# Performance work log

Measured on AMD Instinct MI355X. Metric: run time of the kernel, lower is better.

## Reference

```python
import jax, jax.numpy as jnp
import numpy as np

L, T, H, F = 16, 2048, 2048, 512  # layers, tokens (B*S=16*128), hidden, features


def setup_inputs() -> dict:
    key = jax.random.key(0)
    k1, k2, k3 = jax.random.split(key, 3)
    x = jax.random.normal(k1, (L, T, H), dtype=jnp.float32)          # stacked residual activations
    W_enc = jax.random.normal(k2, (L, F, H), dtype=jnp.float32) * 0.02  # per-layer encoder (out,in)
    # Dense pack of decoders: W_dec[s, t] is the (source s -> target t) decoder weight (H, F).
    # Only entries with s <= t exist in the original ModuleDict; others are masked to zero in reference().
    W_dec = jax.random.normal(k3, (L, L, H, F), dtype=jnp.float32) * 0.02
    return {"x": x, "W_enc": W_enc, "W_dec": W_dec}


def reference(x, W_enc, W_dec):
    n_layers = x.shape[0]
    # encode: feature_activations[l] = JumpReLU(x[l] @ W_enc[l].T), threshold=0 -> relu
    feats = jax.nn.relu(jnp.einsum('sth,sfh->stf', x, W_enc))  # [L, T, F]
    # causal mask over (source s, target l): decoder exists iff s <= l
    tri = jnp.tril(jnp.ones((n_layers, n_layers), x.dtype))     # tri[l, s] = 1 if s <= l
    Wd = W_dec * tri.T[:, :, None, None]                        # zero out s > l entries
    # reconstruction[l] = sum_{s<=l} feats[s] @ W_dec[s,l].T  (single blocked contraction)
    recon = jnp.einsum('stf,slhf->lth', feats, Wd)              # [L, T, H]
    return feats, recon
```

## Files before the change

kernel.cpp:

```cpp
#include <hip/hip_runtime.h>

#define NL 16
#define NT 2048
#define NH 2048
#define NF 512
#define NPAIR 136

typedef short bf16x8 __attribute__((ext_vector_type(8)));
typedef float f32x4 __attribute__((ext_vector_type(4)));
typedef short s16x4 __attribute__((ext_vector_type(4)));

__device__ __forceinline__ short f2bf(float f) {
  union { float f; unsigned u; } x; x.f = f;
  unsigned r = (x.u + 0x7fffu + ((x.u >> 16) & 1u)) >> 16;
  return (short)r;
}


__global__ void k_cvt_f32_bf16(const float* __restrict__ src, short* __restrict__ dst, int n4) {
  int i = blockIdx.x * blockDim.x + threadIdx.x;
  const int stride = gridDim.x * blockDim.x;
  for (; i < n4; i += stride) {
    const float4 v = reinterpret_cast<const float4*>(src)[i];
    s16x4 o;
    o[0] = f2bf(v.x); o[1] = f2bf(v.y); o[2] = f2bf(v.z); o[3] = f2bf(v.w);
    reinterpret_cast<s16x4*>(dst)[i] = o;
  }
}

__global__ void k_cvt_wdec(const float* __restrict__ wdec, short* __restrict__ dst) {
  const int p = blockIdx.y;
  int l = 0;
  while ((l + 1) * (l + 2) / 2 <= p) ++l;
  const int s = p - l * (l + 1) / 2;
  const float* src = wdec + (size_t)(s * NL + l) * (NH * NF);
  short* d = dst + (size_t)p * (NH * NF);
  const int n4 = NH * NF / 4;
  for (int i = blockIdx.x * blockDim.x + threadIdx.x; i < n4; i += gridDim.x * blockDim.x) {
    const float4 v = reinterpret_cast<const float4*>(src)[i];
    s16x4 o;
    o[0] = f2bf(v.x); o[1] = f2bf(v.y); o[2] = f2bf(v.z); o[3] = f2bf(v.w);
    reinterpret_cast<s16x4*>(d)[i] = o;
  }
}


__device__ __forceinline__ void stage64(const short* gtile, int ld, short* lds, int wave, int lane) {
#pragma unroll
  for (int i = 0; i < 4; ++i) {
    const int row = i * 32 + wave * 8 + (lane >> 3);
    const int col = (lane & 7) * 8;
    __builtin_amdgcn_global_load_lds(
        (const __attribute__((address_space(1))) void*)(gtile + (size_t)row * ld + col),
        (__attribute__((address_space(3))) void*)(lds + i * 2048 + wave * 512),
        16, 0, 0);
  }
}

__device__ __forceinline__ void mma_step(const short* As, const short* Bs,
                                         f32x4 acc[4][4], int wr, int wc, int lane) {
  const int r = lane & 15;
  const int ko = (lane >> 4) * 8;
#pragma unroll
  for (int kk = 0; kk < 2; ++kk) {
    bf16x8 a[4], b[4];
#pragma unroll
    for (int m = 0; m < 4; ++m)
      a[m] = *reinterpret_cast<const bf16x8*>(As + (wr * 64 + m * 16 + r) * 64 + kk * 32 + ko);
#pragma unroll
    for (int n = 0; n < 4; ++n)
      b[n] = *reinterpret_cast<const bf16x8*>(Bs + (wc * 64 + n * 16 + r) * 64 + kk * 32 + ko);
#pragma unroll
    for (int m = 0; m < 4; ++m)
#pragma unroll
      for (int n = 0; n < 4; ++n)
        acc[m][n] = __builtin_amdgcn_mfma_f32_16x16x32_bf16(a[m], b[n], acc[m][n], 0, 0, 0);
  }
}


__global__ __launch_bounds__(256, 2) void k_encode(const short* __restrict__ xbf,
                                                   const short* __restrict__ webf,
                                                   float* __restrict__ feats_f32,
                                                   short* __restrict__ feats_bf) {
  __shared__ short As[128 * 64];
  __shared__ short Bs[128 * 64];
  const int l = blockIdx.z;
  const int row0 = blockIdx.y * 128;
  const int col0 = blockIdx.x * 128;
  const int tid = threadIdx.x;
  const int wave = tid >> 6, lane = tid & 63;
  const int wr = wave >> 1, wc = wave & 1;

  const short* A = xbf + (size_t)l * NT * NH + (size_t)row0 * NH;
  const short* B = webf + (size_t)l * NF * NH + (size_t)col0 * NH;

  f32x4 acc[4][4];
#pragma unroll
  for (int m = 0; m < 4; ++m)
#pragma unroll
    for (int n = 0; n < 4; ++n) {
      f32x4 z = {0.f, 0.f, 0.f, 0.f};
      acc[m][n] = z;
    }

  for (int kt = 0; kt < NH / 64; ++kt) {
    stage64(A + kt * 64, NH, As, wave, lane);
    stage64(B + kt * 64, NH, Bs, wave, lane);
    __syncthreads();
    mma_step(As, Bs, acc, wr, wc, lane);
    __syncthreads();
  }

  const int lr = (lane >> 4) * 4, lc = lane & 15;
  float* outF = feats_f32 + (size_t)l * NT * NF;
  short* outB = feats_bf + (size_t)l * NT * NF;
#pragma unroll
  for (int m = 0; m < 4; ++m) {
#pragma unroll
    for (int n = 0; n < 4; ++n) {
#pragma unroll
      for (int rg = 0; rg < 4; ++rg) {
        const int rr = row0 + wr * 64 + m * 16 + lr + rg;
        const int cc = col0 + wc * 64 + n * 16 + lc;
        float v = acc[m][n][rg];
        v = v > 0.f ? v : 0.f;
        outF[(size_t)rr * NF + cc] = v;
        outB[(size_t)rr * NF + cc] = f2bf(v);
      }
    }
  }
}


__global__ __launch_bounds__(256, 2) void k_decode(const short* __restrict__ featsbf,
                                                   const short* __restrict__ wdbf,
                                                   float* __restrict__ recon) {
  __shared__ short As[128 * 64];
  __shared__ short Bs[128 * 64];
  const int l = (NL - 1) - blockIdx.z;
  const int row0 = blockIdx.y * 128;
  const int col0 = blockIdx.x * 128;
  const int tid = threadIdx.x;
  const int wave = tid >> 6, lane = tid & 63;
  const int wr = wave >> 1, wc = wave & 1;

  f32x4 acc[4][4];
#pragma unroll
  for (int m = 0; m < 4; ++m)
#pragma unroll
    for (int n = 0; n < 4; ++n) {
      f32x4 z = {0.f, 0.f, 0.f, 0.f};
      acc[m][n] = z;
    }

  const int KT = 8 * (l + 1);
  const int pbase = l * (l + 1) / 2;

  for (int kt = 0; kt < KT; ++kt) {
    const int s = kt >> 3;
    const int f0 = (kt & 7) * 64;
    const short* At = featsbf + (size_t)s * NT * NF + (size_t)row0 * NF + f0;
    const short* Bt = wdbf + (size_t)(pbase + s) * NH * NF + (size_t)col0 * NF + f0;
    stage64(At, NF, As, wave, lane);
    stage64(Bt, NF, Bs, wave, lane);
    __syncthreads();
    mma_step(As, Bs, acc, wr, wc, lane);
    __syncthreads();
  }

  const int lr = (lane >> 4) * 4, lc = lane & 15;
  float* out = recon + (size_t)l * NT * NH;
#pragma unroll
  for (int m = 0; m < 4; ++m) {
#pragma unroll
    for (int n = 0; n < 4; ++n) {
#pragma unroll
      for (int rg = 0; rg < 4; ++rg) {
        const int rr = row0 + wr * 64 + m * 16 + lr + rg;
        const int cc = col0 + wc * 64 + n * 16 + lc;
        out[(size_t)rr * NH + cc] = acc[m][n][rg];
      }
    }
  }
}


extern "C" void kernel_launch(void* const* d_in, const int* in_sizes, int n_in,
                              void* d_out, int out_size, void* d_ws, size_t ws_size,
                              hipStream_t stream) {
  const float* x = (const float*)d_in[0];
  const float* wenc = (const float*)d_in[1];
  const float* wdec = (const float*)d_in[2];

  float* feats_f32 = (float*)d_out;
  float* recon = feats_f32 + (size_t)NL * NT * NF;

  short* x_bf = (short*)d_ws;
  short* we_bf = x_bf + (size_t)NL * NT * NH;
  short* wd_bf = we_bf + (size_t)NL * NF * NH;
  short* ft_bf = wd_bf + (size_t)NPAIR * NH * NF;

  k_cvt_f32_bf16<<<2048, 256, 0, stream>>>(x, x_bf, NL * NT * NH / 4);
  k_cvt_f32_bf16<<<2048, 256, 0, stream>>>(wenc, we_bf, NL * NF * NH / 4);
  k_cvt_wdec<<<dim3(512, NPAIR), 256, 0, stream>>>(wdec, wd_bf);

  k_encode<<<dim3(NF / 128, NT / 128, NL), 256, 0, stream>>>(x_bf, we_bf, feats_f32, ft_bf);
  k_decode<<<dim3(NH / 128, NT / 128, NL), 256, 0, stream>>>(ft_bf, wd_bf, recon);
}
```

Baseline: 961.1 us.

## Use 256x256 tiles with double-buffered swizzled LDS pipeline for encode/decode GEMMs

```diff
diff --git a/kernel.cpp b/kernel.cpp
--- a/kernel.cpp
+++ b/kernel.cpp
@@ -15,6 +15,8 @@
   unsigned r = (x.u + 0x7fffu + ((x.u >> 16) & 1u)) >> 16;
   return (short)r;
 }
+
+__device__ __forceinline__ int imin(int a, int b) { return a < b ? a : b; }
 
 
 __global__ void k_cvt_f32_bf16(const float* __restrict__ src, short* __restrict__ dst, int n4) {
@@ -45,144 +47,216 @@
 }
 
 
-__device__ __forceinline__ void stage64(const short* gtile, int ld, short* lds, int wave, int lane) {
-#pragma unroll
-  for (int i = 0; i < 4; ++i) {
-    const int row = i * 32 + wave * 8 + (lane >> 3);
-    const int col = (lane & 7) * 8;
+__device__ __forceinline__ bf16x8 lds_frag(const short* slot, int r, int cbyte) {
+  int byte = (r << 7) + cbyte;
+  byte ^= (r & 7) << 4;
+  return *reinterpret_cast<const bf16x8*>(reinterpret_cast<const char*>(slot) + byte);
+}
+
+__device__ __forceinline__ void stage_half(short* slot, const short* gbase, int ld,
+                                           int isA, int h, int tid, int wave) {
+#pragma unroll
+  for (int j = 0; j < 2; ++j) {
+    const int o = j * 8192 + tid * 16;
+    const int r = o >> 7;
+    const int cb = (o ^ ((r & 7) << 4)) & 127;
+    const int g = isA ? (((r >> 6) << 7) + h * 64 + (r & 63))
+                      : (((r >> 5) << 6) + h * 32 + (r & 31));
     __builtin_amdgcn_global_load_lds(
-        (const __attribute__((address_space(1))) void*)(gtile + (size_t)row * ld + col),
-        (__attribute__((address_space(3))) void*)(lds + i * 2048 + wave * 512),
+        (const __attribute__((address_space(1))) void*)(gbase + (size_t)g * ld + (cb >> 1)),
+        (__attribute__((address_space(3))) void*)((char*)slot + j * 8192 + wave * 1024),
         16, 0, 0);
   }
 }
 
-__device__ __forceinline__ void mma_step(const short* As, const short* Bs,
-                                         f32x4 acc[4][4], int wr, int wc, int lane) {
-  const int r = lane & 15;
-  const int ko = (lane >> 4) * 8;
+template <int QA, int QB, typename StageFn>
+__device__ __forceinline__ void phase(short (*bufc)[8192], f32x4 (&acc)[2][2][4][2],
+                                      int wr, int wc, int lane, StageFn stage) {
+  const int lr = lane & 15;
+  const int ko = (lane >> 4) * 16;
+  bf16x8 af[2][4];
+  bf16x8 bfr[2][2];
 #pragma unroll
   for (int kk = 0; kk < 2; ++kk) {
-    bf16x8 a[4], b[4];
 #pragma unroll
     for (int m = 0; m < 4; ++m)
-      a[m] = *reinterpret_cast<const bf16x8*>(As + (wr * 64 + m * 16 + r) * 64 + kk * 32 + ko);
-#pragma unroll
-    for (int n = 0; n < 4; ++n)
-      b[n] = *reinterpret_cast<const bf16x8*>(Bs + (wc * 64 + n * 16 + r) * 64 + kk * 32 + ko);
+      af[kk][m] = lds_frag(bufc[QA], wr * 64 + m * 16 + lr, kk * 64 + ko);
+#pragma unroll
+    for (int n = 0; n < 2; ++n)
+      bfr[kk][n] = lds_frag(bufc[2 + QB], wc * 32 + n * 16 + lr, kk * 64 + ko);
+  }
+  stage();
+  __builtin_amdgcn_s_barrier();
+  __builtin_amdgcn_s_setprio(1);
+#pragma unroll
+  for (int kk = 0; kk < 2; ++kk)
 #pragma unroll
     for (int m = 0; m < 4; ++m)
 #pragma unroll
-      for (int n = 0; n < 4; ++n)
-        acc[m][n] = __builtin_amdgcn_mfma_f32_16x16x32_bf16(a[m], b[n], acc[m][n], 0, 0, 0);
-  }
-}
-
-
-__global__ __launch_bounds__(256, 2) void k_encode(const short* __restrict__ xbf,
+      for (int n = 0; n < 2; ++n)
+        acc[QA][QB][m][n] = __builtin_amdgcn_mfma_f32_16x16x32_bf16(
+            af[kk][m], bfr[kk][n], acc[QA][QB][m][n], 0, 0, 0);
+  __builtin_amdgcn_s_setprio(0);
+  asm volatile("s_waitcnt vmcnt(8)" ::: "memory");
+  __builtin_amdgcn_s_barrier();
+}
+
+
+__global__ __launch_bounds__(512) void k_encode256(const short* __restrict__ xbf,
                                                    const short* __restrict__ webf,
                                                    float* __restrict__ feats_f32,
                                                    short* __restrict__ feats_bf) {
-  __shared__ short As[128 * 64];
-  __shared__ short Bs[128 * 64];
+  __shared__ short lds[2][4][8192];
   const int l = blockIdx.z;
-  const int row0 = blockIdx.y * 128;
-  const int col0 = blockIdx.x * 128;
+  const int row0 = blockIdx.y * 256;
+  const int col0 = blockIdx.x * 256;
   const int tid = threadIdx.x;
   const int wave = tid >> 6, lane = tid & 63;
-  const int wr = wave >> 1, wc = wave & 1;
+  const int wr = wave >> 2, wc = wave & 3;
 
   const short* A = xbf + (size_t)l * NT * NH + (size_t)row0 * NH;
   const short* B = webf + (size_t)l * NF * NH + (size_t)col0 * NH;
 
-  f32x4 acc[4][4];
-#pragma unroll
-  for (int m = 0; m < 4; ++m)
-#pragma unroll
-    for (int n = 0; n < 4; ++n) {
-      f32x4 z = {0.f, 0.f, 0.f, 0.f};
-      acc[m][n] = z;
-    }
-
-  for (int kt = 0; kt < NH / 64; ++kt) {
-    stage64(A + kt * 64, NH, As, wave, lane);
-    stage64(B + kt * 64, NH, Bs, wave, lane);
-    __syncthreads();
-    mma_step(As, Bs, acc, wr, wc, lane);
-    __syncthreads();
-  }
-
-  const int lr = (lane >> 4) * 4, lc = lane & 15;
+  f32x4 acc[2][2][4][2];
+#pragma unroll
+  for (int qa = 0; qa < 2; ++qa)
+#pragma unroll
+    for (int qb = 0; qb < 2; ++qb)
+#pragma unroll
+      for (int m = 0; m < 4; ++m)
+#pragma unroll
+        for (int n = 0; n < 2; ++n) {
+          f32x4 z = {0.f, 0.f, 0.f, 0.f};
+          acc[qa][qb][m][n] = z;
+        }
+
+  const int KT = NH / 64;
+  stage_half(lds[0][0], A, NH, 1, 0, tid, wave);
+  stage_half(lds[0][2], B, NH, 0, 0, tid, wave);
+  stage_half(lds[0][1], A, NH, 1, 1, tid, wave);
+  stage_half(lds[0][3], B, NH, 0, 1, tid, wave);
+  stage_half(lds[1][0], A + 64, NH, 1, 0, tid, wave);
+  stage_half(lds[1][2], B + 64, NH, 0, 0, tid, wave);
+  asm volatile("s_waitcnt vmcnt(4)" ::: "memory");
+  __builtin_amdgcn_s_barrier();
+
+  for (int u = 0; u < KT; ++u) {
+    short(*bufc)[8192] = lds[u & 1];
+    short(*bufn)[8192] = lds[(u + 1) & 1];
+    phase<0, 0>(bufc, acc, wr, wc, lane, [&] {
+      stage_half(bufn[3], B + imin(u + 1, KT - 1) * 64, NH, 0, 1, tid, wave);
+    });
+    phase<0, 1>(bufc, acc, wr, wc, lane, [&] {
+      stage_half(bufn[1], A + imin(u + 1, KT - 1) * 64, NH, 1, 1, tid, wave);
+    });
+    phase<1, 0>(bufc, acc, wr, wc, lane, [&] {
+      stage_half(bufc[0], A + imin(u + 2, KT - 1) * 64, NH, 1, 0, tid, wave);
+    });
+    phase<1, 1>(bufc, acc, wr, wc, lane, [&] {
+      stage_half(bufc[2], B + imin(u + 2, KT - 1) * 64, NH, 0, 0, tid, wave);
+    });
+  }
+
+  const int lr4 = (lane >> 4) * 4, lc = lane & 15;
   float* outF = feats_f32 + (size_t)l * NT * NF;
   short* outB = feats_bf + (size_t)l * NT * NF;
 #pragma unroll
-  for (int m = 0; m < 4; ++m) {
-#pragma unroll
-    for (int n = 0; n < 4; ++n) {
-#pragma unroll
-      for (int rg = 0; rg < 4; ++rg) {
-        const int rr = row0 + wr * 64 + m * 16 + lr + rg;
-        const int cc = col0 + wc * 64 + n * 16 + lc;
-        float v = acc[m][n][rg];
-        v = v > 0.f ? v : 0.f;
-        outF[(size_t)rr * NF + cc] = v;
-        outB[(size_t)rr * NF + cc] = f2bf(v);
-      }
-    }
-  }
-}
-
-
-__global__ __launch_bounds__(256, 2) void k_decode(const short* __restrict__ featsbf,
+  for (int qa = 0; qa < 2; ++qa)
+#pragma unroll
+    for (int qb = 0; qb < 2; ++qb)
+#pragma unroll
+      for (int m = 0; m < 4; ++m)
+#pragma unroll
+        for (int n = 0; n < 2; ++n)
+#pragma unroll
+          for (int rg = 0; rg < 4; ++rg) {
+            const int rr = row0 + wr * 128 + qa * 64 + m * 16 + lr4 + rg;
+            const int cc = col0 + wc * 64 + qb * 32 + n * 16 + lc;
+            float v = acc[qa][qb][m][n][rg];
+            v = v > 0.f ? v : 0.f;
+            outF[(size_t)rr * NF + cc] = v;
+            outB[(size_t)rr * NF + cc] = f2bf(v);
+          }
+}
+
+
+__global__ __launch_bounds__(512) void k_decode256(const short* __restrict__ featsbf,
                                                    const short* __restrict__ wdbf,
                                                    float* __restrict__ recon) {
-  __shared__ short As[128 * 64];
-  __shared__ short Bs[128 * 64];
-  const int l = (NL - 1) - blockIdx.z;
-  const int row0 = blockIdx.y * 128;
-  const int col0 = blockIdx.x * 128;
+  __shared__ short lds[2][4][8192];
+  const int zg = blockIdx.z >> 2, zi = blockIdx.z & 3;
+  const int l = (zi < 2) ? (15 - 2 * zg - zi) : (2 * zg + 3 - zi);
+  const int row0 = blockIdx.y * 256;
+  const int col0 = blockIdx.x * 256;
   const int tid = threadIdx.x;
   const int wave = tid >> 6, lane = tid & 63;
-  const int wr = wave >> 1, wc = wave & 1;
-
-  f32x4 acc[4][4];
-#pragma unroll
-  for (int m = 0; m < 4; ++m)
-#pragma unroll
-    for (int n = 0; n < 4; ++n) {
-      f32x4 z = {0.f, 0.f, 0.f, 0.f};
-      acc[m][n] = z;
-    }
+  const int wr = wave >> 2, wc = wave & 3;
+  const int pbase = l * (l + 1) / 2;
+
+  const short* Af = featsbf + (size_t)row0 * NF;
+  const short* Bw = wdbf + (size_t)col0 * NF;
+
+  f32x4 acc[2][2][4][2];
+#pragma unroll
+  for (int qa = 0; qa < 2; ++qa)
+#pragma unroll
+    for (int qb = 0; qb < 2; ++qb)
+#pragma unroll
+      for (int m = 0; m < 4; ++m)
+#pragma unroll
+        for (int n = 0; n < 2; ++n) {
+          f32x4 z = {0.f, 0.f, 0.f, 0.f};
+          acc[qa][qb][m][n] = z;
+        }
 
   const int KT = 8 * (l + 1);
-  const int pbase = l * (l + 1) / 2;
-
-  for (int kt = 0; kt < KT; ++kt) {
-    const int s = kt >> 3;
-    const int f0 = (kt & 7) * 64;
-    const short* At = featsbf + (size_t)s * NT * NF + (size_t)row0 * NF + f0;
-    const short* Bt = wdbf + (size_t)(pbase + s) * NH * NF + (size_t)col0 * NF + f0;
-    stage64(At, NF, As, wave, lane);
-    stage64(Bt, NF, Bs, wave, lane);
-    __syncthreads();
-    mma_step(As, Bs, acc, wr, wc, lane);
-    __syncthreads();
-  }
-
-  const int lr = (lane >> 4) * 4, lc = lane & 15;
+#define ABASE(kt) (Af + (size_t)((kt) >> 3) * (NT * NF) + ((kt)&7) * 64)
+#define BBASE(kt) (Bw + (size_t)(pbase + ((kt) >> 3)) * (NH * NF) + ((kt)&7) * 64)
+
+  stage_half(lds[0][0], ABASE(0), NF, 1, 0, tid, wave);
+  stage_half(lds[0][2], BBASE(0), NF, 0, 0, tid, wave);
+  stage_half(lds[0][1], ABASE(0), NF, 1, 1, tid, wave);
+  stage_half(lds[0][3], BBASE(0), NF, 0, 1, tid, wave);
+  stage_half(lds[1][0], ABASE(1), NF, 1, 0, tid, wave);
+  stage_half(lds[1][2], BBASE(1), NF, 0, 0, tid, wave);
+  asm volatile("s_waitcnt vmcnt(4)" ::: "memory");
+  __builtin_amdgcn_s_barrier();
+
+  for (int u = 0; u < KT; ++u) {
+    short(*bufc)[8192] = lds[u & 1];
+    short(*bufn)[8192] = lds[(u + 1) & 1];
+    phase<0, 0>(bufc, acc, wr, wc, lane, [&] {
+      stage_half(bufn[3], BBASE(imin(u + 1, KT - 1)), NF, 0, 1, tid, wave);
+    });
+    phase<0, 1>(bufc, acc, wr, wc, lane, [&] {
+      stage_half(bufn[1], ABASE(imin(u + 1, KT - 1)), NF, 1, 1, tid, wave);
+    });
+    phase<1, 0>(bufc, acc, wr, wc, lane, [&] {
+      stage_half(bufc[0], ABASE(imin(u + 2, KT - 1)), NF, 1, 0, tid, wave);
+    });
+    phase<1, 1>(bufc, acc, wr, wc, lane, [&] {
+      stage_half(bufc[2], BBASE(imin(u + 2, KT - 1)), NF, 0, 0, tid, wave);
+    });
+  }
+#undef ABASE
+#undef BBASE
+
+  const int lr4 = (lane >> 4) * 4, lc = lane & 15;
   float* out = recon + (size_t)l * NT * NH;
 #pragma unroll
-  for (int m = 0; m < 4; ++m) {
-#pragma unroll
-    for (int n = 0; n < 4; ++n) {
-#pragma unroll
-      for (int rg = 0; rg < 4; ++rg) {
-        const int rr = row0 + wr * 64 + m * 16 + lr + rg;
-        const int cc = col0 + wc * 64 + n * 16 + lc;
-        out[(size_t)rr * NH + cc] = acc[m][n][rg];
-      }
-    }
-  }
+  for (int qa = 0; qa < 2; ++qa)
+#pragma unroll
+    for (int qb = 0; qb < 2; ++qb)
+#pragma unroll
+      for (int m = 0; m < 4; ++m)
+#pragma unroll
+        for (int n = 0; n < 2; ++n)
+#pragma unroll
+          for (int rg = 0; rg < 4; ++rg) {
+            const int rr = row0 + wr * 128 + qa * 64 + m * 16 + lr4 + rg;
+            const int cc = col0 + wc * 64 + qb * 32 + n * 16 + lc;
+            out[(size_t)rr * NH + cc] = acc[qa][qb][m][n][rg];
+          }
 }
 
 
@@ -205,6 +279,6 @@
   k_cvt_f32_bf16<<<2048, 256, 0, stream>>>(wenc, we_bf, NL * NF * NH / 4);
   k_cvt_wdec<<<dim3(512, NPAIR), 256, 0, stream>>>(wdec, wd_bf);
 
-  k_encode<<<dim3(NF / 128, NT / 128, NL), 256, 0, stream>>>(x_bf, we_bf, feats_f32, ft_bf);
-  k_decode<<<dim3(NH / 128, NT / 128, NL), 256, 0, stream>>>(ft_bf, wd_bf, recon);
-}
+  k_encode256<<<dim3(2, 8, 16), 512, 0, stream>>>(x_bf, we_bf, feats_f32, ft_bf);
+  k_decode256<<<dim3(8, 8, 16), 512, 0, stream>>>(ft_bf, wd_bf, recon);
+}
```

Measured after the change: 911.8 us. 1.05x faster.

## Use 256x256 tiles with 32x32 MFMA and a multi-stage LDS prefetch ring

Applied to the files above, without the earlier changes.

```diff
diff --git a/kernel.cpp b/kernel.cpp
--- a/kernel.cpp
+++ b/kernel.cpp
@@ -7,7 +7,7 @@
 #define NPAIR 136
 
 typedef short bf16x8 __attribute__((ext_vector_type(8)));
-typedef float f32x4 __attribute__((ext_vector_type(4)));
+typedef float f32x16 __attribute__((ext_vector_type(16)));
 typedef short s16x4 __attribute__((ext_vector_type(4)));
 
 __device__ __forceinline__ short f2bf(float f) {
@@ -15,6 +15,8 @@
   unsigned r = (x.u + 0x7fffu + ((x.u >> 16) & 1u)) >> 16;
   return (short)r;
 }
+
+__device__ __forceinline__ int imin(int a, int b) { return a < b ? a : b; }
 
 
 __global__ void k_cvt_f32_bf16(const float* __restrict__ src, short* __restrict__ dst, int n4) {
@@ -45,144 +47,172 @@
 }
 
 
-__device__ __forceinline__ void stage64(const short* gtile, int ld, short* lds, int wave, int lane) {
-#pragma unroll
-  for (int i = 0; i < 4; ++i) {
-    const int row = i * 32 + wave * 8 + (lane >> 3);
-    const int col = (lane & 7) * 8;
+__device__ __forceinline__ bf16x8 frag32(const short* slot, int row, int kbyte) {
+  const int byte = (row << 6) + (kbyte ^ ((row & 3) << 4));
+  return *reinterpret_cast<const bf16x8*>(reinterpret_cast<const char*>(slot) + byte);
+}
+
+__device__ __forceinline__ void stage32(short* slot, const short* gbase, int ld,
+                                        int tid, int wave) {
+#pragma unroll
+  for (int j = 0; j < 2; ++j) {
+    const int o = j * 8192 + tid * 16;
+    const int r = o >> 6;
+    const int cb = (o & 63) ^ ((r & 3) << 4);
     __builtin_amdgcn_global_load_lds(
-        (const __attribute__((address_space(1))) void*)(gtile + (size_t)row * ld + col),
-        (__attribute__((address_space(3))) void*)(lds + i * 2048 + wave * 512),
+        (const __attribute__((address_space(1))) void*)(gbase + (size_t)r * ld + (cb >> 1)),
+        (__attribute__((address_space(3))) void*)((char*)slot + j * 8192 + wave * 1024),
         16, 0, 0);
   }
 }
 
-__device__ __forceinline__ void mma_step(const short* As, const short* Bs,
-                                         f32x4 acc[4][4], int wr, int wc, int lane) {
-  const int r = lane & 15;
-  const int ko = (lane >> 4) * 8;
-#pragma unroll
-  for (int kk = 0; kk < 2; ++kk) {
-    bf16x8 a[4], b[4];
-#pragma unroll
-    for (int m = 0; m < 4; ++m)
-      a[m] = *reinterpret_cast<const bf16x8*>(As + (wr * 64 + m * 16 + r) * 64 + kk * 32 + ko);
-#pragma unroll
-    for (int n = 0; n < 4; ++n)
-      b[n] = *reinterpret_cast<const bf16x8*>(Bs + (wc * 64 + n * 16 + r) * 64 + kk * 32 + ko);
-#pragma unroll
-    for (int m = 0; m < 4; ++m)
-#pragma unroll
-      for (int n = 0; n < 4; ++n)
-        acc[m][n] = __builtin_amdgcn_mfma_f32_16x16x32_bf16(a[m], b[n], acc[m][n], 0, 0, 0);
-  }
-}
-
-
-__global__ __launch_bounds__(256, 2) void k_encode(const short* __restrict__ xbf,
-                                                   const short* __restrict__ webf,
-                                                   float* __restrict__ feats_f32,
-                                                   short* __restrict__ feats_bf) {
-  __shared__ short As[128 * 64];
-  __shared__ short Bs[128 * 64];
+template <typename SFn>
+__device__ __forceinline__ void ktile32(const short (*buf)[8192], f32x16 (&acc)[4][2],
+                                        int wr, int wc, int lane, SFn stagefn) {
+  stagefn();
+  const int rl = lane & 31;
+  const int khi = (lane >> 5) * 16;
+  bf16x8 a[2][4], b[2][2];
+#pragma unroll
+  for (int ks = 0; ks < 2; ++ks) {
+#pragma unroll
+    for (int tm = 0; tm < 4; ++tm)
+      a[ks][tm] = frag32(buf[0], wr * 128 + tm * 32 + rl, ks * 32 + khi);
+#pragma unroll
+    for (int tn = 0; tn < 2; ++tn)
+      b[ks][tn] = frag32(buf[1], wc * 64 + tn * 32 + rl, ks * 32 + khi);
+  }
+  __builtin_amdgcn_s_setprio(1);
+#pragma unroll
+  for (int ks = 0; ks < 2; ++ks)
+#pragma unroll
+    for (int tm = 0; tm < 4; ++tm)
+#pragma unroll
+      for (int tn = 0; tn < 2; ++tn)
+        acc[tm][tn] = __builtin_amdgcn_mfma_f32_32x32x16_bf16(a[ks][tm], b[ks][tn],
+                                                              acc[tm][tn], 0, 0, 0);
+  __builtin_amdgcn_s_setprio(0);
+  asm volatile("s_waitcnt vmcnt(8) lgkmcnt(0)" ::: "memory");
+  __builtin_amdgcn_s_barrier();
+}
+
+
+__global__ __launch_bounds__(512, 2) void k_encode256(const short* __restrict__ xbf,
+                                                      const short* __restrict__ webf,
+                                                      float* __restrict__ feats_f32,
+                                                      short* __restrict__ feats_bf) {
+  __shared__ short lds[4][2][8192];
   const int l = blockIdx.z;
-  const int row0 = blockIdx.y * 128;
-  const int col0 = blockIdx.x * 128;
+  const int row0 = blockIdx.y * 256;
+  const int col0 = blockIdx.x * 256;
   const int tid = threadIdx.x;
   const int wave = tid >> 6, lane = tid & 63;
-  const int wr = wave >> 1, wc = wave & 1;
+  const int wr = wave >> 2, wc = wave & 3;
 
   const short* A = xbf + (size_t)l * NT * NH + (size_t)row0 * NH;
   const short* B = webf + (size_t)l * NF * NH + (size_t)col0 * NH;
 
-  f32x4 acc[4][4];
-#pragma unroll
-  for (int m = 0; m < 4; ++m)
-#pragma unroll
-    for (int n = 0; n < 4; ++n) {
-      f32x4 z = {0.f, 0.f, 0.f, 0.f};
-      acc[m][n] = z;
-    }
-
-  for (int kt = 0; kt < NH / 64; ++kt) {
-    stage64(A + kt * 64, NH, As, wave, lane);
-    stage64(B + kt * 64, NH, Bs, wave, lane);
-    __syncthreads();
-    mma_step(As, Bs, acc, wr, wc, lane);
-    __syncthreads();
-  }
-
-  const int lr = (lane >> 4) * 4, lc = lane & 15;
+  f32x16 acc[4][2];
+#pragma unroll
+  for (int tm = 0; tm < 4; ++tm)
+#pragma unroll
+    for (int tn = 0; tn < 2; ++tn)
+#pragma unroll
+      for (int q = 0; q < 16; ++q) acc[tm][tn][q] = 0.f;
+
+  const int KT = NH / 32;
+#pragma unroll
+  for (int t = 0; t < 3; ++t) {
+    stage32(lds[t][0], A + t * 32, NH, tid, wave);
+    stage32(lds[t][1], B + t * 32, NH, tid, wave);
+  }
+  asm volatile("s_waitcnt vmcnt(8)" ::: "memory");
+  __builtin_amdgcn_s_barrier();
+
+  for (int u = 0; u < KT; ++u) {
+    ktile32(lds[u & 3], acc, wr, wc, lane, [&] {
+      const int t = imin(u + 3, KT - 1);
+      stage32(lds[(u + 3) & 3][0], A + t * 32, NH, tid, wave);
+      stage32(lds[(u + 3) & 3][1], B + t * 32, NH, tid, wave);
+    });
+  }
+
+  const int rl = lane & 31, lhi = (lane >> 5) * 4;
   float* outF = feats_f32 + (size_t)l * NT * NF;
   short* outB = feats_bf + (size_t)l * NT * NF;
 #pragma unroll
-  for (int m = 0; m < 4; ++m) {
-#pragma unroll
-    for (int n = 0; n < 4; ++n) {
-#pragma unroll
-      for (int rg = 0; rg < 4; ++rg) {
-        const int rr = row0 + wr * 64 + m * 16 + lr + rg;
-        const int cc = col0 + wc * 64 + n * 16 + lc;
-        float v = acc[m][n][rg];
+  for (int tm = 0; tm < 4; ++tm)
+#pragma unroll
+    for (int tn = 0; tn < 2; ++tn)
+#pragma unroll
+      for (int q = 0; q < 16; ++q) {
+        const int rr = row0 + wr * 128 + tm * 32 + (q & 3) + 8 * (q >> 2) + lhi;
+        const int cc = col0 + wc * 64 + tn * 32 + rl;
+        float v = acc[tm][tn][q];
         v = v > 0.f ? v : 0.f;
         outF[(size_t)rr * NF + cc] = v;
         outB[(size_t)rr * NF + cc] = f2bf(v);
       }
-    }
-  }
-}
-
-
-__global__ __launch_bounds__(256, 2) void k_decode(const short* __restrict__ featsbf,
-                                                   const short* __restrict__ wdbf,
-                                                   float* __restrict__ recon) {
-  __shared__ short As[128 * 64];
-  __shared__ short Bs[128 * 64];
+}
+
+
+__global__ __launch_bounds__(512, 2) void k_decode256(const short* __restrict__ featsbf,
+                                                      const short* __restrict__ wdbf,
+                                                      float* __restrict__ recon) {
+  __shared__ short lds[4][2][8192];
   const int l = (NL - 1) - blockIdx.z;
-  const int row0 = blockIdx.y * 128;
-  const int col0 = blockIdx.x * 128;
+  const int row0 = blockIdx.y * 256;
+  const int col0 = blockIdx.x * 256;
   const int tid = threadIdx.x;
   const int wave = tid >> 6, lane = tid & 63;
-  const int wr = wave >> 1, wc = wave & 1;
-
-  f32x4 acc[4][4];
-#pragma unroll
-  for (int m = 0; m < 4; ++m)
-#pragma unroll
-    for (int n = 0; n < 4; ++n) {
-      f32x4 z = {0.f, 0.f, 0.f, 0.f};
-      acc[m][n] = z;
-    }
-
-  const int KT = 8 * (l + 1);
+  const int wr = wave >> 2, wc = wave & 3;
   const int pbase = l * (l + 1) / 2;
 
-  for (int kt = 0; kt < KT; ++kt) {
-    const int s = kt >> 3;
-    const int f0 = (kt & 7) * 64;
-    const short* At = featsbf + (size_t)s * NT * NF + (size_t)row0 * NF + f0;
-    const short* Bt = wdbf + (size_t)(pbase + s) * NH * NF + (size_t)col0 * NF + f0;
-    stage64(At, NF, As, wave, lane);
-    stage64(Bt, NF, Bs, wave, lane);
-    __syncthreads();
-    mma_step(As, Bs, acc, wr, wc, lane);
-    __syncthreads();
-  }
-
-  const int lr = (lane >> 4) * 4, lc = lane & 15;
+  const short* Af = featsbf + (size_t)row0 * NF;
+  const short* Bw = wdbf + (size_t)col0 * NF;
+
+  f32x16 acc[4][2];
+#pragma unroll
+  for (int tm = 0; tm < 4; ++tm)
+#pragma unroll
+    for (int tn = 0; tn < 2; ++tn)
+#pragma unroll
+      for (int q = 0; q < 16; ++q) acc[tm][tn][q] = 0.f;
+
+  const int KT = 16 * (l + 1);
+#define ABASE(t) (Af + (size_t)((t) >> 4) * (NT * NF) + ((t)&15) * 32)
+#define BBASE(t) (Bw + (size_t)(pbase + ((t) >> 4)) * (NH * NF) + ((t)&15) * 32)
+
+#pragma unroll
+  for (int t = 0; t < 3; ++t) {
+    stage32(lds[t][0], ABASE(t), NF, tid, wave);
+    stage32(lds[t][1], BBASE(t), NF, tid, wave);
+  }
+  asm volatile("s_waitcnt vmcnt(8)" ::: "memory");
+  __builtin_amdgcn_s_barrier();
+
+  for (int u = 0; u < KT; ++u) {
+    ktile32(lds[u & 3], acc, wr, wc, lane, [&] {
+      const int t = imin(u + 3, KT - 1);
+      stage32(lds[(u + 3) & 3][0], ABASE(t), NF, tid, wave);
+      stage32(lds[(u + 3) & 3][1], BBASE(t), NF, tid, wave);
+    });
+  }
+#undef ABASE
+#undef BBASE
+
+  const int rl = lane & 31, lhi = (lane >> 5) * 4;
   float* out = recon + (size_t)l * NT * NH;
 #pragma unroll
-  for (int m = 0; m < 4; ++m) {
-#pragma unroll
-    for (int n = 0; n < 4; ++n) {
-#pragma unroll
-      for (int rg = 0; rg < 4; ++rg) {
-        const int rr = row0 + wr * 64 + m * 16 + lr + rg;
-        const int cc = col0 + wc * 64 + n * 16 + lc;
-        out[(size_t)rr * NH + cc] = acc[m][n][rg];
+  for (int tm = 0; tm < 4; ++tm)
+#pragma unroll
+    for (int tn = 0; tn < 2; ++tn)
+#pragma unroll
+      for (int q = 0; q < 16; ++q) {
+        const int rr = row0 + wr * 128 + tm * 32 + (q & 3) + 8 * (q >> 2) + lhi;
+        const int cc = col0 + wc * 64 + tn * 32 + rl;
+        out[(size_t)rr * NH + cc] = acc[tm][tn][q];
       }
-    }
-  }
 }
 
 
@@ -205,6 +235,6 @@
   k_cvt_f32_bf16<<<2048, 256, 0, stream>>>(wenc, we_bf, NL * NF * NH / 4);
   k_cvt_wdec<<<dim3(512, NPAIR), 256, 0, stream>>>(wdec, wd_bf);
 
-  k_encode<<<dim3(NF / 128, NT / 128, NL), 256, 0, stream>>>(x_bf, we_bf, feats_f32, ft_bf);
-  k_decode<<<dim3(NH / 128, NT / 128, NL), 256, 0, stream>>>(ft_bf, wd_bf, recon);
-}
+  k_encode256<<<dim3(2, 8, 16), 512, 0, stream>>>(x_bf, we_bf, feats_f32, ft_bf);
+  k_decode256<<<dim3(8, 8, 16), 512, 0, stream>>>(ft_bf, wd_bf, recon);
+}
```

Result: slower. 994.5 us (+3.5%).
